# Optimization experiments

Measured on AMD Instinct MI355X. Metric: run time of the kernel, lower is better.

## Reference

```python
import jax, jax.numpy as jnp
import numpy as np

N_HEADS = 8
EPS = 1e-5


def setup_inputs() -> dict:
    key = jax.random.key(0)
    ks = jax.random.split(key, 5)
    B, C, H, W = 4, 512, 64, 64
    X = jax.random.normal(ks[0], (B, C, H, W), dtype=jnp.float32)
    gamma = jnp.ones((C,), dtype=jnp.float32)
    beta = jnp.zeros((C,), dtype=jnp.float32)
    Wqkv = jax.random.normal(ks[1], (3 * C, C), dtype=jnp.float32) * 0.02
    bqkv = jnp.zeros((3 * C,), dtype=jnp.float32)
    Wproj = jax.random.normal(ks[2], (C, C), dtype=jnp.float32) * 0.02
    bproj = jnp.zeros((C,), dtype=jnp.float32)
    return {"X": X, "gamma": gamma, "beta": beta, "Wqkv": Wqkv, "bqkv": bqkv,
            "Wproj": Wproj, "bproj": bproj}


def reference(X, gamma, beta, Wqkv, bqkv, Wproj, bproj):
    B, C, H, W = X.shape
    hw = H * W
    d3 = (3 * C) // N_HEADS  # 3*d_head per-head latent (QKV interleaved per head)
    scale = jnp.sqrt(jnp.asarray(C / N_HEADS, dtype=X.dtype))
    # (B, C, H, W) -> (B, hw, C)
    t = X.reshape(B, C, hw).transpose(0, 2, 1)
    # LayerNorm over channels
    mu = jnp.mean(t, axis=-1, keepdims=True)
    var = jnp.var(t, axis=-1, keepdims=True)
    t = (t - mu) * jax.lax.rsqrt(var + EPS) * gamma + beta
    # qkv linear: (B, hw, 3C)
    t = t @ Wqkv.T + bqkv
    # einops 'batch hw (heads latent) -> (batch heads) hw latent'
    t = t.reshape(B, hw, N_HEADS, d3).transpose(0, 2, 1, 3)  # (B, heads, hw, 3*d_head)
    Q, K, V = jnp.split(t, 3, axis=-1)  # each (B, heads, hw, d_head)
    S = jnp.einsum('bhqd,bhkd->bhqk', Q, K) / scale
    A = jax.nn.softmax(S, axis=-1)
    O = jnp.einsum('bhqk,bhkd->bhqd', A, V)  # (B, heads, hw, d_head)
    O = O.transpose(0, 2, 1, 3).reshape(B, hw, C)
    O = O @ Wproj.T + bproj
    return O.transpose(0, 2, 1).reshape(B, C, H, W)
```

## Files before the change

kernel.cpp:

```cpp
#include <hip/hip_runtime.h>
#include <hip/hip_bf16.h>

typedef __bf16 bf16_t;
typedef __attribute__((ext_vector_type(8))) __bf16 bf16x8;
typedef __attribute__((ext_vector_type(4))) __bf16 bf16x4;
typedef __attribute__((ext_vector_type(4))) float f32x4;

#define MFMA16(A, B, C) __builtin_amdgcn_mfma_f32_16x16x32_bf16((A), (B), (C), 0, 0, 0)

#if __has_builtin(__builtin_amdgcn_exp2f)
#define EXP2F(x) __builtin_amdgcn_exp2f(x)
#else
#define EXP2F(x) exp2f(x)
#endif

#define QSCALE 0.1803368801111244f

__global__ __launch_bounds__(256) void cvt_kernel(const float* __restrict__ Wq,
                                                  const float* __restrict__ Wp,
                                                  bf16_t* __restrict__ qh,
                                                  bf16_t* __restrict__ ql,
                                                  bf16_t* __restrict__ ph,
                                                  bf16_t* __restrict__ pl) {
  const int i = (blockIdx.x * 256 + threadIdx.x) * 4;
  if (i < 786432) {
    const float4 v = *(const float4*)(Wq + i);
    const float vv[4] = {v.x, v.y, v.z, v.w};
    bf16x4 h, l;
    #pragma unroll
    for (int j = 0; j < 4; ++j) {
      h[j] = (bf16_t)vv[j];
      l[j] = (bf16_t)(vv[j] - (float)h[j]);
    }
    *(bf16x4*)(qh + i) = h;
    *(bf16x4*)(ql + i) = l;
  } else {
    const int j0 = i - 786432;
    const float4 v = *(const float4*)(Wp + j0);
    const float vv[4] = {v.x, v.y, v.z, v.w};
    bf16x4 h, l;
    #pragma unroll
    for (int j = 0; j < 4; ++j) {
      h[j] = (bf16_t)vv[j];
      l[j] = (bf16_t)(vv[j] - (float)h[j]);
    }
    *(bf16x4*)(ph + j0) = h;
    *(bf16x4*)(pl + j0) = l;
  }
}

__global__ __launch_bounds__(256) void ln_kernel(const float* __restrict__ X,
                                                 const float* __restrict__ gamma,
                                                 const float* __restrict__ beta,
                                                 bf16_t* __restrict__ Th,
                                                 bf16_t* __restrict__ Tl) {
  __shared__ __align__(16) bf16_t tile[512 * 32];
  __shared__ float red1[8][32];
  __shared__ float red2[8][32];
  __shared__ float smu[32], srs[32];
  __shared__ float sg[512], sb[512];
  const int tid = threadIdx.x;
  const int g = tid >> 5, pi = tid & 31;
  const int b = blockIdx.y;
  const int p0 = blockIdx.x * 32;
  sg[tid] = gamma[tid];
  sg[tid + 256] = gamma[tid + 256];
  sb[tid] = beta[tid];
  sb[tid + 256] = beta[tid + 256];
  const float* Xb = X + ((size_t)b * 512) * 4096 + p0;
  float s1 = 0.f, s2 = 0.f;
  #pragma unroll 4
  for (int c = g * 64; c < g * 64 + 64; ++c) {
    const float x = Xb[(size_t)c * 4096 + pi];
    tile[c * 32 + pi] = (bf16_t)x;
    s1 += x;
    s2 += x * x;
  }
  red1[g][pi] = s1;
  red2[g][pi] = s2;
  __syncthreads();
  if (tid < 32) {
    float a = 0.f, q = 0.f;
    #pragma unroll
    for (int k = 0; k < 8; ++k) {
      a += red1[k][tid];
      q += red2[k][tid];
    }
    const float mu = a * (1.f / 512.f);
    const float var = q * (1.f / 512.f) - mu * mu;
    smu[tid] = mu;
    srs[tid] = rsqrtf(var + 1e-5f);
  }
  __syncthreads();
  const int pi2 = tid >> 3, qq = tid & 7;
  const float mu = smu[pi2], rs = srs[pi2];
  const size_t outoff = ((size_t)(b * 4096 + p0 + pi2)) * 512;
  #pragma unroll
  for (int ii = 0; ii < 8; ++ii) {
    const int c0 = qq * 64 + ii * 8;
    bf16x8 ph, pl;
    #pragma unroll
    for (int j = 0; j < 8; ++j) {
      const float x = (float)tile[(c0 + j) * 32 + pi2];
      const float y = (x - mu) * rs * sg[c0 + j] + sb[c0 + j];
      const bf16_t hi = (bf16_t)y;
      ph[j] = hi;
      pl[j] = (bf16_t)(y - (float)hi);
    }
    *(bf16x8*)(Th + outoff + c0) = ph;
    *(bf16x8*)(Tl + outoff + c0) = pl;
  }
}

__global__ __launch_bounds__(256) void gemm_qkv(const bf16_t* __restrict__ Wqh,
                                                const bf16_t* __restrict__ Wql,
                                                const bf16_t* __restrict__ Th,
                                                const bf16_t* __restrict__ Tl,
                                                const float* __restrict__ bqkv,
                                                bf16_t* __restrict__ QKV) {
  extern __shared__ char smem[];
  char* const Ah = smem;
  char* const Al = smem + 16384;
  char* const Bh = smem + 32768;
  char* const Bl = smem + 49152;
  const int pos0 = blockIdx.x * 128;
  const int oc0 = blockIdx.y * 128;
  const int tid = threadIdx.x;
  const int l = tid & 63, w = tid >> 6;
  const int wr = w >> 1, wc = w & 1;
  f32x4 acc[4][4] = {};
  for (int kt = 0; kt < 512; kt += 64) {
    __syncthreads();
    #pragma unroll
    for (int i = 0; i < 4; ++i) {
      const int chunk = tid + 256 * i;
      const int row = chunk >> 3;
      const int cp = (chunk & 7) ^ (row & 7);
      const size_t offA = (size_t)(oc0 + row) * 512 + kt + cp * 8;
      const size_t offB = (size_t)(pos0 + row) * 512 + kt + cp * 8;
      __builtin_amdgcn_global_load_lds(
          (const __attribute__((address_space(1))) void*)(Wqh + offA),
          (__attribute__((address_space(3))) void*)(Ah + chunk * 16), 16, 0, 0);
      __builtin_amdgcn_global_load_lds(
          (const __attribute__((address_space(1))) void*)(Wql + offA),
          (__attribute__((address_space(3))) void*)(Al + chunk * 16), 16, 0, 0);
      __builtin_amdgcn_global_load_lds(
          (const __attribute__((address_space(1))) void*)(Th + offB),
          (__attribute__((address_space(3))) void*)(Bh + chunk * 16), 16, 0, 0);
      __builtin_amdgcn_global_load_lds(
          (const __attribute__((address_space(1))) void*)(Tl + offB),
          (__attribute__((address_space(3))) void*)(Bl + chunk * 16), 16, 0, 0);
    }
    __syncthreads();
    #pragma unroll
    for (int ks = 0; ks < 2; ++ks) {
      bf16x8 ah[4], al[4], bh[4], bl[4];
      #pragma unroll
      for (int mt = 0; mt < 4; ++mt) {
        const int row = wr * 64 + mt * 16 + (l & 15);
        const int off = row * 128 + ((ks * 64 + (l >> 4) * 16) ^ ((row & 7) << 4));
        ah[mt] = *(const bf16x8*)(Ah + off);
        al[mt] = *(const bf16x8*)(Al + off);
      }
      #pragma unroll
      for (int nt = 0; nt < 4; ++nt) {
        const int row = wc * 64 + nt * 16 + (l & 15);
        const int off = row * 128 + ((ks * 64 + (l >> 4) * 16) ^ ((row & 7) << 4));
        bh[nt] = *(const bf16x8*)(Bh + off);
        bl[nt] = *(const bf16x8*)(Bl + off);
      }
      #pragma unroll
      for (int mt = 0; mt < 4; ++mt)
        #pragma unroll
        for (int nt = 0; nt < 4; ++nt) {
          acc[mt][nt] = MFMA16(ah[mt], bh[nt], acc[mt][nt]);
          acc[mt][nt] = MFMA16(ah[mt], bl[nt], acc[mt][nt]);
          acc[mt][nt] = MFMA16(al[mt], bh[nt], acc[mt][nt]);
        }
    }
  }
  #pragma unroll
  for (int mt = 0; mt < 4; ++mt) {
    const int ocb = oc0 + wr * 64 + mt * 16 + 4 * (l >> 4);
    const float4 bias = *(const float4*)(bqkv + ocb);
    const float qs = ((ocb % 192) < 64) ? QSCALE : 1.0f;
    #pragma unroll
    for (int nt = 0; nt < 4; ++nt) {
      const int pos = pos0 + wc * 64 + nt * 16 + (l & 15);
      bf16x4 o;
      o[0] = (bf16_t)((acc[mt][nt][0] + bias.x) * qs);
      o[1] = (bf16_t)((acc[mt][nt][1] + bias.y) * qs);
      o[2] = (bf16_t)((acc[mt][nt][2] + bias.z) * qs);
      o[3] = (bf16_t)((acc[mt][nt][3] + bias.w) * qs);
      *(bf16x4*)(QKV + (size_t)pos * 1536 + ocb) = o;
    }
  }
}

__global__ __launch_bounds__(256) void attn_kernel(const bf16_t* __restrict__ QKV,
                                                   bf16_t* __restrict__ Oh,
                                                   bf16_t* __restrict__ Ol) {
  const int o = blockIdx.x;
  const int sid = (o & 7) * 128 + (o >> 3);
  const int qt = sid & 31;
  const int bh = sid >> 5;
  const int b = bh >> 3, h = bh & 7;
  const int tid = threadIdx.x;
  const int l = tid & 63, w = tid >> 6;
  const int lg = l >> 4, lr = l & 15;

  __shared__ __align__(16) bf16_t KsA[64 * 64];
  __shared__ __align__(16) bf16_t KsB[64 * 64];
  __shared__ __align__(16) bf16_t Vt[64 * 64];
  __shared__ __align__(16) bf16_t Ps[4][32 * 64];

  const bf16_t* base = QKV + (size_t)(b * 4096) * 1536 + h * 192;
  const bf16_t* kbase = base + 64;
  const bf16_t* vbase = base + 128;
  const int q0 = qt * 128 + w * 32;

  bf16x8 qf[2][2];
  #pragma unroll
  for (int mq = 0; mq < 2; ++mq)
    #pragma unroll
    for (int ks = 0; ks < 2; ++ks)
      qf[mq][ks] = *(const bf16x8*)(base + (size_t)(q0 + mq * 16 + lr) * 1536 +
                                    ks * 32 + 8 * lg);

  bf16x8 onesb;
  {
    const bf16_t one = (bf16_t)1.0f;
    #pragma unroll
    for (int j = 0; j < 8; ++j) onesb[j] = one;
  }

  f32x4 acc_o[2][4] = {};
  f32x4 acc_d[2] = {};
  char* const psw = (char*)&Ps[w][0];

  auto stageK = [&](bf16_t* dst, int k0) {
    #pragma unroll
    for (int i = 0; i < 2; ++i) {
      const int c = tid + 256 * i;
      const int row = c >> 3;
      const int cp = (c & 7) ^ (row & 7);
      const bf16_t* g = kbase + (size_t)(k0 + row) * 1536 + cp * 8;
      __builtin_amdgcn_global_load_lds(
          (const __attribute__((address_space(1))) void*)g,
          (__attribute__((address_space(3))) void*)((char*)dst + c * 16), 16, 0, 0);
    }
  };
  auto loadV = [&](int k0, bf16x8& v0, bf16x8& v1) {
    const bf16_t* vs = vbase + (size_t)(k0 + l) * 1536 + w * 16;
    v0 = *(const bf16x8*)vs;
    v1 = *(const bf16x8*)(vs + 8);
  };
  auto writeV = [&](bf16x8 v0, bf16x8 v1) {
    char* const vt = (char*)Vt;
    #pragma unroll
    for (int j = 0; j < 8; ++j) {
      const int d0 = w * 16 + j, d1 = w * 16 + 8 + j;
      *(bf16_t*)(vt + d0 * 128 + ((2 * l) ^ ((d0 & 7) << 4))) = v0[j];
      *(bf16_t*)(vt + d1 * 128 + ((2 * l) ^ ((d1 & 7) << 4))) = v1[j];
    }
  };
  auto compute = [&](const bf16_t* Kbuf) {
    f32x4 st[4][2] = {};
    __builtin_amdgcn_s_setprio(1);
    #pragma unroll
    for (int ks = 0; ks < 2; ++ks) {
      bf16x8 kb[4];
      #pragma unroll
      for (int kt = 0; kt < 4; ++kt) {
        const int row = kt * 16 + lr;
        kb[kt] = *(const bf16x8*)((const char*)Kbuf + row * 128 +
                                  ((ks * 64 + lg * 16) ^ ((row & 7) << 4)));
      }
      #pragma unroll
      for (int kt = 0; kt < 4; ++kt) {
        st[kt][0] = MFMA16(kb[kt], qf[0][ks], st[kt][0]);
        st[kt][1] = MFMA16(kb[kt], qf[1][ks], st[kt][1]);
      }
    }
    __builtin_amdgcn_s_setprio(0);
    #pragma unroll
    for (int mq = 0; mq < 2; ++mq) {
      const int prow = mq * 16 + lr;
      const int rs = (prow & 7) << 4;
      #pragma unroll
      for (int kt = 0; kt < 4; ++kt) {
        bf16x4 pk;
        pk[0] = (bf16_t)EXP2F(st[kt][mq][0]);
        pk[1] = (bf16_t)EXP2F(st[kt][mq][1]);
        pk[2] = (bf16_t)EXP2F(st[kt][mq][2]);
        pk[3] = (bf16_t)EXP2F(st[kt][mq][3]);
        *(bf16x4*)(psw + prow * 128 + ((kt * 32 + lg * 8) ^ rs)) = pk;
      }
    }
    #pragma unroll
    for (int ks = 0; ks < 2; ++ks) {
      bf16x8 pa[2], vb[4];
      #pragma unroll
      for (int mt = 0; mt < 2; ++mt) {
        const int row = mt * 16 + lr;
        pa[mt] = *(const bf16x8*)(psw + row * 128 +
                                  ((ks * 64 + lg * 16) ^ ((row & 7) << 4)));
      }
      #pragma unroll
      for (int dt = 0; dt < 4; ++dt) {
        const int row = dt * 16 + lr;
        vb[dt] = *(const bf16x8*)((const char*)Vt + row * 128 +
                                  ((ks * 64 + lg * 16) ^ ((row & 7) << 4)));
      }
      __builtin_amdgcn_s_setprio(1);
      #pragma unroll
      for (int mt = 0; mt < 2; ++mt) {
        #pragma unroll
        for (int dt = 0; dt < 4; ++dt)
          acc_o[mt][dt] = MFMA16(pa[mt], vb[dt], acc_o[mt][dt]);
        acc_d[mt] = MFMA16(pa[mt], onesb, acc_d[mt]);
      }
      __builtin_amdgcn_s_setprio(0);
    }
  };

  stageK(KsA, 0);
  bf16x8 va0, va1, vb0, vb1;
  loadV(0, va0, va1);

  for (int t = 0; t < 64; t += 2) {
    __syncthreads();
    writeV(va0, va1);
    __syncthreads();
    stageK(KsB, (t + 1) * 64);
    loadV((t + 1) * 64, vb0, vb1);
    compute(KsA);

    __syncthreads();
    writeV(vb0, vb1);
    __syncthreads();
    if (t + 2 < 64) {
      stageK(KsA, (t + 2) * 64);
      loadV((t + 2) * 64, va0, va1);
    }
    compute(KsB);
  }

  #pragma unroll
  for (int mt = 0; mt < 2; ++mt) {
    #pragma unroll
    for (int r = 0; r < 4; ++r) {
      const float inv = 1.f / acc_d[mt][r];
      const int row = mt * 16 + 4 * lg + r;
      const int rsw = (row & 7) << 4;
      #pragma unroll
      for (int dt = 0; dt < 4; ++dt) {
        const float v = acc_o[mt][dt][r] * inv;
        acc_o[mt][dt][r] = v;
        const int col = dt * 16 + lr;
        *(bf16_t*)(psw + ((row * 128 + col * 2) ^ rsw)) = (bf16_t)v;
      }
    }
  }
  const int row2 = l & 31, hf = l >> 5;
  {
    bf16_t* orow = Oh + (size_t)(b * 4096 + q0 + row2) * 512 + h * 64 + hf * 32;
    #pragma unroll
    for (int c = 0; c < 4; ++c) {
      const bf16x8 vv =
          *(const bf16x8*)(psw + ((row2 * 128 + hf * 64 + c * 16) ^ ((row2 & 7) << 4)));
      *(bf16x8*)(orow + c * 8) = vv;
    }
  }
  #pragma unroll
  for (int mt = 0; mt < 2; ++mt) {
    #pragma unroll
    for (int r = 0; r < 4; ++r) {
      const int row = mt * 16 + 4 * lg + r;
      const int rsw = (row & 7) << 4;
      #pragma unroll
      for (int dt = 0; dt < 4; ++dt) {
        const float v = acc_o[mt][dt][r];
        const bf16_t hi = (bf16_t)v;
        const bf16_t lo = (bf16_t)(v - (float)hi);
        const int col = dt * 16 + lr;
        *(bf16_t*)(psw + ((row * 128 + col * 2) ^ rsw)) = lo;
      }
    }
  }
  {
    bf16_t* orow = Ol + (size_t)(b * 4096 + q0 + row2) * 512 + h * 64 + hf * 32;
    #pragma unroll
    for (int c = 0; c < 4; ++c) {
      const bf16x8 vv =
          *(const bf16x8*)(psw + ((row2 * 128 + hf * 64 + c * 16) ^ ((row2 & 7) << 4)));
      *(bf16x8*)(orow + c * 8) = vv;
    }
  }
}

__global__ __launch_bounds__(256) void gemm_proj(const bf16_t* __restrict__ Oh,
                                                 const bf16_t* __restrict__ Ol,
                                                 const bf16_t* __restrict__ Wph,
                                                 const bf16_t* __restrict__ Wpl,
                                                 const float* __restrict__ bproj,
                                                 float* __restrict__ Y) {
  extern __shared__ char smem[];
  char* const Ah = smem;
  char* const Al = smem + 16384;
  char* const Bh = smem + 32768;
  char* const Bl = smem + 49152;
  const int pos0 = blockIdx.y * 128;
  const int oc0 = blockIdx.x * 128;
  const int tid = threadIdx.x;
  const int l = tid & 63, w = tid >> 6;
  const int wr = w >> 1, wc = w & 1;
  f32x4 acc[4][4] = {};
  for (int kt = 0; kt < 512; kt += 64) {
    __syncthreads();
    #pragma unroll
    for (int i = 0; i < 4; ++i) {
      const int chunk = tid + 256 * i;
      const int row = chunk >> 3;
      const int cp = (chunk & 7) ^ (row & 7);
      const size_t offA = (size_t)(pos0 + row) * 512 + kt + cp * 8;
      const size_t offB = (size_t)(oc0 + row) * 512 + kt + cp * 8;
      __builtin_amdgcn_global_load_lds(
          (const __attribute__((address_space(1))) void*)(Oh + offA),
          (__attribute__((address_space(3))) void*)(Ah + chunk * 16), 16, 0, 0);
      __builtin_amdgcn_global_load_lds(
          (const __attribute__((address_space(1))) void*)(Ol + offA),
          (__attribute__((address_space(3))) void*)(Al + chunk * 16), 16, 0, 0);
      __builtin_amdgcn_global_load_lds(
          (const __attribute__((address_space(1))) void*)(Wph + offB),
          (__attribute__((address_space(3))) void*)(Bh + chunk * 16), 16, 0, 0);
      __builtin_amdgcn_global_load_lds(
          (const __attribute__((address_space(1))) void*)(Wpl + offB),
          (__attribute__((address_space(3))) void*)(Bl + chunk * 16), 16, 0, 0);
    }
    __syncthreads();
    #pragma unroll
    for (int ks = 0; ks < 2; ++ks) {
      bf16x8 ah[4], al[4], bh[4], bl[4];
      #pragma unroll
      for (int mt = 0; mt < 4; ++mt) {
        const int row = wr * 64 + mt * 16 + (l & 15);
        const int off = row * 128 + ((ks * 64 + (l >> 4) * 16) ^ ((row & 7) << 4));
        ah[mt] = *(const bf16x8*)(Ah + off);
        al[mt] = *(const bf16x8*)(Al + off);
      }
      #pragma unroll
      for (int nt = 0; nt < 4; ++nt) {
        const int row = wc * 64 + nt * 16 + (l & 15);
        const int off = row * 128 + ((ks * 64 + (l >> 4) * 16) ^ ((row & 7) << 4));
        bh[nt] = *(const bf16x8*)(Bh + off);
        bl[nt] = *(const bf16x8*)(Bl + off);
      }
      #pragma unroll
      for (int mt = 0; mt < 4; ++mt)
        #pragma unroll
        for (int nt = 0; nt < 4; ++nt) {
          acc[mt][nt] = MFMA16(ah[mt], bh[nt], acc[mt][nt]);
          acc[mt][nt] = MFMA16(ah[mt], bl[nt], acc[mt][nt]);
          acc[mt][nt] = MFMA16(al[mt], bh[nt], acc[mt][nt]);
        }
    }
  }
  #pragma unroll
  for (int mt = 0; mt < 4; ++mt) {
    const int posb = pos0 + wr * 64 + mt * 16 + 4 * (l >> 4);
    const int bb_ = posb >> 12, p = posb & 4095;
    #pragma unroll
    for (int nt = 0; nt < 4; ++nt) {
      const int oc = oc0 + wc * 64 + nt * 16 + (l & 15);
      const float bias = bproj[oc];
      float4 v;
      v.x = acc[mt][nt][0] + bias;
      v.y = acc[mt][nt][1] + bias;
      v.z = acc[mt][nt][2] + bias;
      v.w = acc[mt][nt][3] + bias;
      *(float4*)(Y + ((size_t)(bb_ * 512 + oc)) * 4096 + p) = v;
    }
  }
}

extern "C" void kernel_launch(void* const* d_in, const int* in_sizes, int n_in,
                              void* d_out, int out_size, void* d_ws, size_t ws_size,
                              hipStream_t stream) {
  const float* X = (const float*)d_in[0];
  const float* gamma = (const float*)d_in[1];
  const float* beta = (const float*)d_in[2];
  const float* Wqkv = (const float*)d_in[3];
  const float* bqkv = (const float*)d_in[4];
  const float* Wproj = (const float*)d_in[5];
  const float* bproj = (const float*)d_in[6];
  float* Y = (float*)d_out;
  char* ws = (char*)d_ws;

  bf16_t* Wq_hi = (bf16_t*)(ws + 0);
  bf16_t* Wq_lo = (bf16_t*)(ws + 1572864);
  bf16_t* Wp_hi = (bf16_t*)(ws + 3145728);
  bf16_t* Wp_lo = (bf16_t*)(ws + 3670016);
  bf16_t* T_hi = (bf16_t*)(ws + 4194304);
  bf16_t* T_lo = (bf16_t*)(ws + 20971520);
  bf16_t* QKVb = (bf16_t*)(ws + 37748736);
  bf16_t* O_hi = T_hi;
  bf16_t* O_lo = T_lo;

  cvt_kernel<<<1024, 256, 0, stream>>>(Wqkv, Wproj, Wq_hi, Wq_lo, Wp_hi, Wp_lo);
  ln_kernel<<<dim3(128, 4), 256, 0, stream>>>(X, gamma, beta, T_hi, T_lo);
  gemm_qkv<<<dim3(128, 12), 256, 65536, stream>>>(Wq_hi, Wq_lo, T_hi, T_lo, bqkv, QKVb);
  attn_kernel<<<dim3(1024), 256, 0, stream>>>(QKVb, O_hi, O_lo);
  gemm_proj<<<dim3(4, 128), 256, 65536, stream>>>(O_hi, O_lo, Wp_hi, Wp_lo, bproj, Y);
}
```

Measured before the change: 437.9 us.

## Enlarge attention blocks to 512 threads and double-buffer V tiles

Measured after the change: 402.5 us. -8.1%, faster.

```diff
diff --git a/kernel.cpp b/kernel.cpp
--- a/kernel.cpp
+++ b/kernel.cpp
@@ -197,13 +197,13 @@
   }
 }
 
-__global__ __launch_bounds__(256) void attn_kernel(const bf16_t* __restrict__ QKV,
+__global__ __launch_bounds__(512) void attn_kernel(const bf16_t* __restrict__ QKV,
                                                    bf16_t* __restrict__ Oh,
                                                    bf16_t* __restrict__ Ol) {
   const int o = blockIdx.x;
-  const int sid = (o & 7) * 128 + (o >> 3);
-  const int qt = sid & 31;
-  const int bh = sid >> 5;
+  const int sid = (o & 7) * 64 + (o >> 3);
+  const int qt = sid & 15;
+  const int bh = sid >> 4;
   const int b = bh >> 3, h = bh & 7;
   const int tid = threadIdx.x;
   const int l = tid & 63, w = tid >> 6;
@@ -211,13 +211,14 @@
 
   __shared__ __align__(16) bf16_t KsA[64 * 64];
   __shared__ __align__(16) bf16_t KsB[64 * 64];
-  __shared__ __align__(16) bf16_t Vt[64 * 64];
-  __shared__ __align__(16) bf16_t Ps[4][32 * 64];
+  __shared__ __align__(16) bf16_t VtA[64 * 64];
+  __shared__ __align__(16) bf16_t VtB[64 * 64];
+  __shared__ __align__(16) bf16_t Ps[8][32 * 64];
 
   const bf16_t* base = QKV + (size_t)(b * 4096) * 1536 + h * 192;
   const bf16_t* kbase = base + 64;
   const bf16_t* vbase = base + 128;
-  const int q0 = qt * 128 + w * 32;
+  const int q0 = qt * 256 + w * 32;
 
   bf16x8 qf[2][2];
   #pragma unroll
@@ -239,32 +240,27 @@
   char* const psw = (char*)&Ps[w][0];
 
   auto stageK = [&](bf16_t* dst, int k0) {
-    #pragma unroll
-    for (int i = 0; i < 2; ++i) {
-      const int c = tid + 256 * i;
-      const int row = c >> 3;
-      const int cp = (c & 7) ^ (row & 7);
-      const bf16_t* g = kbase + (size_t)(k0 + row) * 1536 + cp * 8;
-      __builtin_amdgcn_global_load_lds(
-          (const __attribute__((address_space(1))) void*)g,
-          (__attribute__((address_space(3))) void*)((char*)dst + c * 16), 16, 0, 0);
-    }
+    const int row = tid >> 3;
+    const int cp = (tid & 7) ^ (row & 7);
+    const bf16_t* g = kbase + (size_t)(k0 + row) * 1536 + cp * 8;
+    __builtin_amdgcn_global_load_lds(
+        (const __attribute__((address_space(1))) void*)g,
+        (__attribute__((address_space(3))) void*)((char*)dst + tid * 16), 16, 0, 0);
   };
-  auto loadV = [&](int k0, bf16x8& v0, bf16x8& v1) {
-    const bf16_t* vs = vbase + (size_t)(k0 + l) * 1536 + w * 16;
+  auto loadV = [&](int k0, bf16x8& v0) {
+    const bf16_t* vs = vbase + (size_t)(k0 + (tid & 63)) * 1536 + (tid >> 6) * 8;
     v0 = *(const bf16x8*)vs;
-    v1 = *(const bf16x8*)(vs + 8);
   };
-  auto writeV = [&](bf16x8 v0, bf16x8 v1) {
+  auto writeV = [&](bf16_t* Vt, bf16x8 v0) {
     char* const vt = (char*)Vt;
+    const int key = tid & 63;
     #pragma unroll
     for (int j = 0; j < 8; ++j) {
-      const int d0 = w * 16 + j, d1 = w * 16 + 8 + j;
-      *(bf16_t*)(vt + d0 * 128 + ((2 * l) ^ ((d0 & 7) << 4))) = v0[j];
-      *(bf16_t*)(vt + d1 * 128 + ((2 * l) ^ ((d1 & 7) << 4))) = v1[j];
+      const int d = (tid >> 6) * 8 + j;
+      *(bf16_t*)(vt + d * 128 + ((2 * key) ^ ((d & 7) << 4))) = v0[j];
     }
   };
-  auto compute = [&](const bf16_t* Kbuf) {
+  auto compute = [&](const bf16_t* Kbuf, const bf16_t* Vbuf) {
     f32x4 st[4][2] = {};
     __builtin_amdgcn_s_setprio(1);
     #pragma unroll
@@ -309,7 +305,7 @@
       #pragma unroll
       for (int dt = 0; dt < 4; ++dt) {
         const int row = dt * 16 + lr;
-        vb[dt] = *(const bf16x8*)((const char*)Vt + row * 128 +
+        vb[dt] = *(const bf16x8*)((const char*)Vbuf + row * 128 +
                                   ((ks * 64 + lg * 16) ^ ((row & 7) << 4)));
       }
       __builtin_amdgcn_s_setprio(1);
@@ -324,26 +320,25 @@
     }
   };
 
+  bf16x8 va, vb;
   stageK(KsA, 0);
-  bf16x8 va0, va1, vb0, vb1;
-  loadV(0, va0, va1);
+  loadV(0, va);
+  writeV(VtA, va);
 
   for (int t = 0; t < 64; t += 2) {
     __syncthreads();
-    writeV(va0, va1);
-    __syncthreads();
     stageK(KsB, (t + 1) * 64);
-    loadV((t + 1) * 64, vb0, vb1);
-    compute(KsA);
-
-    __syncthreads();
-    writeV(vb0, vb1);
+    loadV((t + 1) * 64, vb);
+    compute(KsA, VtA);
+    writeV(VtB, vb);
+
     __syncthreads();
     if (t + 2 < 64) {
       stageK(KsA, (t + 2) * 64);
-      loadV((t + 2) * 64, va0, va1);
-    }
-    compute(KsB);
+      loadV((t + 2) * 64, va);
+    }
+    compute(KsB, VtB);
+    if (t + 2 < 64) writeV(VtA, va);
   }
 
   #pragma unroll
@@ -510,6 +505,6 @@
   cvt_kernel<<<1024, 256, 0, stream>>>(Wqkv, Wproj, Wq_hi, Wq_lo, Wp_hi, Wp_lo);
   ln_kernel<<<dim3(128, 4), 256, 0, stream>>>(X, gamma, beta, T_hi, T_lo);
   gemm_qkv<<<dim3(128, 12), 256, 65536, stream>>>(Wq_hi, Wq_lo, T_hi, T_lo, bqkv, QKVb);
-  attn_kernel<<<dim3(1024), 256, 0, stream>>>(QKVb, O_hi, O_lo);
+  attn_kernel<<<dim3(512), 512, 0, stream>>>(QKVb, O_hi, O_lo);
   gemm_proj<<<dim3(4, 128), 256, 65536, stream>>>(O_hi, O_lo, Wp_hi, Wp_lo, bproj, Y);
 }
```
